# Kernel tuning notes

Measured on AMD Instinct MI355X. Metric: run time of the kernel, lower is better.

Reference implementation:

```python
import jax, jax.numpy as jnp
import numpy as np

N, D, H, DH, FF, NE, NNZ = 4096, 128, 2, 64, 256, 2048, 65536
EPS = 1e-5

def layer_norm(x, g, b):
    m = jnp.mean(x, axis=-1, keepdims=True)
    v = jnp.var(x, axis=-1, keepdims=True)
    return (x - m) / jnp.sqrt(v + EPS) * g + b

def setup_inputs() -> dict:
    key = jax.random.key(0)
    ks = jax.random.split(key, 24)
    s = 0.05
    node_idx = jax.random.randint(ks[1], (NNZ,), 0, N)
    he_idx = jax.random.randint(ks[2], (NNZ,), 0, NE)
    return {
        "x": jax.random.normal(ks[0], (N, D), dtype=jnp.float32),
        "edge": jnp.stack([node_idx, he_idx]).astype(jnp.int64),
        "Wq": jax.random.normal(ks[3], (D, D)) * s, "bq": jnp.zeros((D,)),
        "Wk": jax.random.normal(ks[4], (D, D)) * s, "bk": jnp.zeros((D,)),
        "Wv": jax.random.normal(ks[5], (D, D)) * s, "bv": jnp.zeros((D,)),
        "Wo": jax.random.normal(ks[6], (D, D)) * s, "bo": jnp.zeros((D,)),
        "g_ln1": jnp.ones((D,)), "b_ln1": jnp.zeros((D,)),
        "W1": jax.random.normal(ks[7], (D, FF)) * s, "bf1": jnp.zeros((FF,)),
        "W2": jax.random.normal(ks[8], (FF, D)) * s, "bf2": jnp.zeros((D,)),
        "g_ln2": jnp.ones((D,)), "b_ln2": jnp.zeros((D,)),
        "Wh": jax.random.normal(ks[9], (D, D)) * s, "bh": jnp.zeros((D,)),
    }

def reference(x, edge, Wq, bq, Wk, bk, Wv, bv, Wo, bo, g_ln1, b_ln1,
              W1, bf1, W2, bf2, g_ln2, b_ln2, Wh, bh):
    # dropout layers run in eval mode (identity) for a deterministic reference
    def mha_block(h):
        q = (h @ Wq + bq).reshape(N, H, DH)
        k = (h @ Wk + bk).reshape(N, H, DH)
        v = (h @ Wv + bv).reshape(N, H, DH)
        scores = jnp.einsum('nhd,mhd->hnm', q, k) / jnp.sqrt(jnp.float32(DH))
        attn = jax.nn.softmax(scores, axis=-1)            # [H,N,N]
        o = jnp.einsum('hnm,mhd->nhd', attn, v).reshape(N, D)
        return layer_norm(h + o @ Wo + bo, g_ln1, b_ln1)

    def ff_block(h):
        z = jax.nn.sigmoid(h @ W1 + bf1)
        return layer_norm(h + z @ W2 + bf2, g_ln2, b_ln2)

    h = ff_block(mha_block(x))
    h = ff_block(mha_block(h))

    # HypergraphConv: out = D^{-1} H B^{-1} H^T (X Theta) + bias
    node_idx = edge[0]
    he_idx = edge[1]
    xt = h @ Wh                                            # [N,D]
    ones = jnp.ones((NNZ,), dtype=xt.dtype)
    Bdeg = jax.ops.segment_sum(ones, he_idx, num_segments=NE)
    Binv = jnp.where(Bdeg > 0, 1.0 / Bdeg, 0.0)
    Ddeg = jax.ops.segment_sum(ones, node_idx, num_segments=N)
    Dinv = jnp.where(Ddeg > 0, 1.0 / Ddeg, 0.0)
    e = jax.ops.segment_sum(xt[node_idx], he_idx, num_segments=NE) * Binv[:, None]
    out = jax.ops.segment_sum(e[he_idx], node_idx, num_segments=N) * Dinv[:, None] + bh
    return jax.nn.relu(out)
```

## Files before the change

### kernel.cpp

```cpp
#include <hip/hip_runtime.h>
#include <hip/hip_bf16.h>
#include <cstddef>

#define N_NODES 4096
#define DIM     128
#define NHEAD   2
#define DHEAD   64
#define FFDIM   256
#define NEDGE   2048
#define NNZ_E   65536
#define NSPLIT  8

typedef __attribute__((ext_vector_type(8))) short bf16x8;
typedef __attribute__((ext_vector_type(4))) float f32x4;
typedef unsigned short u16;

__device__ __forceinline__ u16 f2b(float f) {
    unsigned u = __float_as_uint(f);
    return (u16)((u + 0x7FFFu + ((u >> 16) & 1u)) >> 16);
}
__device__ __forceinline__ float b2f_bits(u16 h) {
    return __uint_as_float(((unsigned)h) << 16);
}

__global__ void prep(const float* __restrict__ x, float* __restrict__ h,
                     u16* __restrict__ hh, u16* __restrict__ hl,
                     const float* W0, const float* W1, const float* W2,
                     const float* W3, const float* W4, const float* W5,
                     const float* W6,
                     u16* P0, u16* P1, u16* P2, u16* P3, u16* P4, u16* P5, u16* P6,
                     int* __restrict__ cnt) {
    const int bx = blockIdx.x;
    if (bx < 2048) {
        int i = bx * 256 + threadIdx.x;
        float f = x[i];
        h[i] = f;
        u16 hi = f2b(f);
        hh[i] = hi;
        hl[i] = f2b(f - b2f_bits(hi));
        return;
    }
    if (bx >= 2944) {
        int i = (bx - 2944) * 256 + threadIdx.x;
        if (i < NEDGE + N_NODES) cnt[i] = 0;
        return;
    }
    const int p = bx - 2048;
    const int sel = p >> 7;
    const float* W; u16* P; int K, NC;
    switch (sel) {
        case 0: W = W0; P = P0; K = 128; NC = 128; break;
        case 1: W = W1; P = P1; K = 128; NC = 128; break;
        case 2: W = W2; P = P2; K = 128; NC = 128; break;
        case 3: W = W3; P = P3; K = 128; NC = 128; break;
        case 4: W = W4; P = P4; K = 128; NC = 128; break;
        case 5: W = W5; P = P5; K = 128; NC = 256; break;
        default: W = W6; P = P6; K = 256; NC = 128; break;
    }
    int i = (p & 127) * 256 + threadIdx.x;
    if (i < K * NC) {
        int k = i / NC, n = i % NC;
        float f = W[i];
        u16 hb = f2b(f);
        size_t o = ((size_t)(k >> 3) * NC + n) * 8 + (k & 7);
        P[o] = hb;
        P[(size_t)K * NC + o] = f2b(f - b2f_bits(hb));
    }
}

template<int K, int NC>
__global__ __launch_bounds__(256) void gemm_mfma(const u16* __restrict__ Ah,
                                                 const u16* __restrict__ Al,
                                                 const u16* __restrict__ Wp,
                                                 float* __restrict__ C0) {
    const int tid = threadIdx.x, w = tid >> 6, lane = tid & 63;
    const int qi = lane & 15, gi = lane >> 4;
    const int row0 = blockIdx.x * 64 + w * 16;
    const int col0 = blockIdx.y * 32;
    const u16* Wlo = Wp + (size_t)K * NC;

    f32x4 acc[2];
    acc[0] = (f32x4){0.f, 0.f, 0.f, 0.f};
    acc[1] = (f32x4){0.f, 0.f, 0.f, 0.f};

#pragma unroll 4
    for (int kc = 0; kc < K / 32; ++kc) {
        const int k0 = kc * 32;
        const size_t ao = (size_t)(row0 + qi) * K + k0 + gi * 8;
        bf16x8 ah = *(const bf16x8*)(Ah + ao);
        bf16x8 al = *(const bf16x8*)(Al + ao);
#pragma unroll
        for (int c = 0; c < 2; ++c) {
            const size_t wo = ((size_t)(k0 / 8 + gi) * NC + col0 + c * 16 + qi) * 8;
            bf16x8 wh = *(const bf16x8*)(Wp + wo);
            bf16x8 wl = *(const bf16x8*)(Wlo + wo);
            acc[c] = __builtin_amdgcn_mfma_f32_16x16x32_bf16(ah, wh, acc[c], 0, 0, 0);
            acc[c] = __builtin_amdgcn_mfma_f32_16x16x32_bf16(al, wh, acc[c], 0, 0, 0);
            acc[c] = __builtin_amdgcn_mfma_f32_16x16x32_bf16(ah, wl, acc[c], 0, 0, 0);
        }
    }

#pragma unroll
    for (int c = 0; c < 2; ++c) {
        const int col = col0 + c * 16 + qi;
#pragma unroll
        for (int r = 0; r < 4; ++r) {
            const int grow = row0 + gi * 4 + r;
            C0[(size_t)grow * NC + col] = acc[c][r];
        }
    }
}

__global__ __launch_bounds__(256) void qkv_mfma(const u16* __restrict__ Ah,
                                                const u16* __restrict__ Al,
                                                const u16* __restrict__ Wq,
                                                const u16* __restrict__ Wk,
                                                const u16* __restrict__ Wv,
                                                const float* __restrict__ bq,
                                                const float* __restrict__ bk,
                                                const float* __restrict__ bv,
                                                u16* __restrict__ qb,
                                                u16* __restrict__ kb,
                                                u16* __restrict__ vtb) {
    const int K = 128, NC = 128;
    const int tid = threadIdx.x, w = tid >> 6, lane = tid & 63;
    const int qi = lane & 15, gi = lane >> 4;
    const int row0 = blockIdx.x * 64 + w * 16;
    const int sel = blockIdx.y >> 2;
    const int col0 = (blockIdx.y & 3) * 32;
    const u16* Wp = (sel == 0) ? Wq : (sel == 1) ? Wk : Wv;
    const float* bias = (sel == 0) ? bq : (sel == 1) ? bk : bv;
    const u16* Wlo = Wp + (size_t)K * NC;

    f32x4 acc[2];
    acc[0] = (f32x4){0.f, 0.f, 0.f, 0.f};
    acc[1] = (f32x4){0.f, 0.f, 0.f, 0.f};

#pragma unroll 4
    for (int kc = 0; kc < K / 32; ++kc) {
        const int k0 = kc * 32;
        const size_t ao = (size_t)(row0 + qi) * K + k0 + gi * 8;
        bf16x8 ah = *(const bf16x8*)(Ah + ao);
        bf16x8 al = *(const bf16x8*)(Al + ao);
#pragma unroll
        for (int c = 0; c < 2; ++c) {
            const size_t wo = ((size_t)(k0 / 8 + gi) * NC + col0 + c * 16 + qi) * 8;
            bf16x8 wh = *(const bf16x8*)(Wp + wo);
            bf16x8 wl = *(const bf16x8*)(Wlo + wo);
            acc[c] = __builtin_amdgcn_mfma_f32_16x16x32_bf16(ah, wh, acc[c], 0, 0, 0);
            acc[c] = __builtin_amdgcn_mfma_f32_16x16x32_bf16(al, wh, acc[c], 0, 0, 0);
            acc[c] = __builtin_amdgcn_mfma_f32_16x16x32_bf16(ah, wl, acc[c], 0, 0, 0);
        }
    }

#pragma unroll
    for (int c = 0; c < 2; ++c) {
        const int col = col0 + c * 16 + qi;
        const int hh = col >> 6, d = col & 63;
        float bv_ = bias[col];
        if (sel < 2) {
            u16* dst = (sel == 0) ? qb : kb;
#pragma unroll
            for (int r = 0; r < 4; ++r) {
                const int grow = row0 + gi * 4 + r;
                dst[((size_t)hh * N_NODES + grow) * 64 + d] = f2b(acc[c][r] + bv_);
            }
        } else {
            const int grow0 = row0 + gi * 4;
            ushort4 pw;
            pw.x = f2b(acc[c][0] + bv_);
            pw.y = f2b(acc[c][1] + bv_);
            pw.z = f2b(acc[c][2] + bv_);
            pw.w = f2b(acc[c][3] + bv_);
            *(ushort4*)&vtb[((size_t)hh * 64 + d) * N_NODES + grow0] = pw;
        }
    }
}

#define ROWP 72
__global__ __launch_bounds__(256) void attn_mfma(const u16* __restrict__ qb,
                                                 const u16* __restrict__ kb,
                                                 const u16* __restrict__ vtb,
                                                 float* __restrict__ op,
                                                 float* __restrict__ mlm,
                                                 float* __restrict__ mll) {
    __shared__ __align__(16) u16 k_s[64 * ROWP];
    __shared__ __align__(16) u16 vt_s[64 * ROWP];
    __shared__ __align__(16) u16 p_s[4][16 * ROWP];
    const int h = blockIdx.y;
    const int s = blockIdx.z;
    const int row0 = blockIdx.x * 64;
    const int tid = threadIdx.x;
    const int w = tid >> 6, lane = tid & 63;
    const int qi = lane & 15, gi = lane >> 4;
    const float CE = 0.18033688011f;

    const u16* qrow = qb + ((size_t)h * N_NODES + row0 + w * 16 + qi) * 64 + gi * 8;
    bf16x8 qf0 = *(const bf16x8*)qrow;
    bf16x8 qf1 = *(const bf16x8*)(qrow + 32);

    f32x4 oc[4];
#pragma unroll
    for (int i = 0; i < 4; ++i) oc[i] = (f32x4){0.f, 0.f, 0.f, 0.f};
    float m_run = -INFINITY, l_run = 0.f;

    const u16* kbh = kb + (size_t)h * N_NODES * 64;
    const u16* vth = vtb + (size_t)h * 64 * N_NODES;

    for (int kt = s * (N_NODES / 64 / NSPLIT); kt < (s + 1) * (N_NODES / 64 / NSPLIT); ++kt) {
        const u16* ksrc = kbh + kt * 64 * 64;
#pragma unroll
        for (int i = 0; i < 2; ++i) {
            int c = tid + i * 256;
            int r = c >> 3, ss = c & 7;
            *(uint4*)&k_s[r * ROWP + ss * 8]  = *(const uint4*)(ksrc + c * 8);
            *(uint4*)&vt_s[r * ROWP + ss * 8] = *(const uint4*)(vth + (size_t)r * N_NODES + kt * 64 + ss * 8);
        }
        __syncthreads();

        f32x4 sc[4];
#pragma unroll
        for (int t = 0; t < 4; ++t) {
            const u16* krow = &k_s[(t * 16 + qi) * ROWP + gi * 8];
            bf16x8 ka0 = *(const bf16x8*)krow;
            bf16x8 ka1 = *(const bf16x8*)(krow + 32);
            f32x4 z = (f32x4){0.f, 0.f, 0.f, 0.f};
            z = __builtin_amdgcn_mfma_f32_16x16x32_bf16(ka0, qf0, z, 0, 0, 0);
            sc[t] = __builtin_amdgcn_mfma_f32_16x16x32_bf16(ka1, qf1, z, 0, 0, 0);
        }

        float smax = -INFINITY;
#pragma unroll
        for (int t = 0; t < 4; ++t)
            smax = fmaxf(smax, fmaxf(fmaxf(sc[t][0], sc[t][1]), fmaxf(sc[t][2], sc[t][3])));
        smax = fmaxf(smax, __shfl_xor(smax, 16));
        smax = fmaxf(smax, __shfl_xor(smax, 32));
        float mn = fmaxf(m_run, smax);
        float alpha = exp2f((m_run - mn) * CE);
        m_run = mn;
        float nb = mn * CE;
        float psum = 0.f;
#pragma unroll
        for (int t = 0; t < 4; ++t) {
            ushort4 pw;
            float p0 = exp2f(fmaf(sc[t][0], CE, -nb)); psum += p0; pw.x = f2b(p0);
            float p1 = exp2f(fmaf(sc[t][1], CE, -nb)); psum += p1; pw.y = f2b(p1);
            float p2 = exp2f(fmaf(sc[t][2], CE, -nb)); psum += p2; pw.z = f2b(p2);
            float p3 = exp2f(fmaf(sc[t][3], CE, -nb)); psum += p3; pw.w = f2b(p3);
            *(ushort4*)&p_s[w][qi * ROWP + t * 16 + gi * 4] = pw;
        }
        psum += __shfl_xor(psum, 16);
        psum += __shfl_xor(psum, 32);
        l_run = l_run * alpha + psum;

        float a0 = __shfl(alpha, gi * 4 + 0);
        float a1 = __shfl(alpha, gi * 4 + 1);
        float a2 = __shfl(alpha, gi * 4 + 2);
        float a3 = __shfl(alpha, gi * 4 + 3);
#pragma unroll
        for (int d = 0; d < 4; ++d) {
            oc[d][0] *= a0; oc[d][1] *= a1; oc[d][2] *= a2; oc[d][3] *= a3;
        }

        const u16* prow = &p_s[w][qi * ROWP];
        bf16x8 pa0 = *(const bf16x8*)(prow + gi * 8);
        bf16x8 pa1 = *(const bf16x8*)(prow + 32 + gi * 8);
#pragma unroll
        for (int d = 0; d < 4; ++d) {
            const u16* vrow = &vt_s[(d * 16 + qi) * ROWP + gi * 8];
            bf16x8 vb0 = *(const bf16x8*)vrow;
            bf16x8 vb1 = *(const bf16x8*)(vrow + 32);
            oc[d] = __builtin_amdgcn_mfma_f32_16x16x32_bf16(pa0, vb0, oc[d], 0, 0, 0);
            oc[d] = __builtin_amdgcn_mfma_f32_16x16x32_bf16(pa1, vb1, oc[d], 0, 0, 0);
        }
        __syncthreads();
    }

    float* opd = op + (size_t)s * N_NODES * 128;
#pragma unroll
    for (int d = 0; d < 4; ++d) {
        size_t cb = h * 64 + d * 16 + qi;
        opd[(size_t)(row0 + w * 16 + gi * 4 + 0) * 128 + cb] = oc[d][0];
        opd[(size_t)(row0 + w * 16 + gi * 4 + 1) * 128 + cb] = oc[d][1];
        opd[(size_t)(row0 + w * 16 + gi * 4 + 2) * 128 + cb] = oc[d][2];
        opd[(size_t)(row0 + w * 16 + gi * 4 + 3) * 128 + cb] = oc[d][3];
    }
    if (gi == 0) {
        size_t mi = (size_t)s * NHEAD * N_NODES + (size_t)h * N_NODES + row0 + w * 16 + qi;
        mlm[mi] = m_run;
        mll[mi] = l_run;
    }
}

#define ROWA 136
#define ROWZ 264
#define ROWH 132
template<int DO_QKV>
__global__ __launch_bounds__(256) void mega_layer(
        const float* __restrict__ op, const float* __restrict__ mlm,
        const float* __restrict__ mll,
        const u16* __restrict__ wp_o, const float* __restrict__ bo,
        float* __restrict__ h,
        const float* __restrict__ g1, const float* __restrict__ b1,
        const u16* __restrict__ wp_1, const float* __restrict__ bf1,
        const u16* __restrict__ wp_2, const float* __restrict__ bf2,
        const float* __restrict__ g2, const float* __restrict__ b2,
        const u16* __restrict__ wp_q, const u16* __restrict__ wp_k,
        const u16* __restrict__ wp_v,
        const float* __restrict__ bq, const float* __restrict__ bk,
        const float* __restrict__ bv,
        u16* __restrict__ qb, u16* __restrict__ kb, u16* __restrict__ vtb) {
    __shared__ __align__(16) u16 zbuf[16 * ROWZ * 2];
    __shared__ __align__(16) u16 hp_hi[16 * ROWA];
    __shared__ __align__(16) u16 hp_lo[16 * ROWA];
    __shared__ float hln[16 * ROWH];
    __shared__ float ws_s[NSPLIT][32];
    __shared__ float Linv_s[32];
    __shared__ float wsum[4][16], wsq[4][16];
    const float CE = 0.18033688011f;
    const int tid = threadIdx.x, w = tid >> 6, lane = tid & 63;
    const int qi = lane & 15, gi = lane >> 4;
    const int row0 = blockIdx.x * 16;
    u16* a_hi = zbuf;
    u16* a_lo = zbuf + 16 * ROWA;
    u16* z_hi = zbuf;
    u16* z_lo = zbuf + 16 * ROWZ;

    if (tid < 32) {
        int r = tid >> 1, hd = tid & 1;
        size_t mb = (size_t)hd * N_NODES + row0 + r;
        float m[NSPLIT], l[NSPLIT], mx = -INFINITY;
#pragma unroll
        for (int s = 0; s < NSPLIT; ++s) {
            m[s] = mlm[mb + (size_t)s * NHEAD * N_NODES];
            l[s] = mll[mb + (size_t)s * NHEAD * N_NODES];
            mx = fmaxf(mx, m[s]);
        }
        float L = 0.f;
#pragma unroll
        for (int s = 0; s < NSPLIT; ++s) {
            float ws = exp2f((m[s] - mx) * CE);
            ws_s[s][tid] = ws;
            L += ws * l[s];
        }
        Linv_s[tid] = 1.f / L;
    }
    __syncthreads();

    for (int e = tid; e < 16 * 128; e += 256) {
        int r = e >> 7, c = e & 127, hd = c >> 6;
        size_t idx = (size_t)(row0 + r) * 128 + c;
        float O = 0.f;
#pragma unroll
        for (int s = 0; s < NSPLIT; ++s)
            O += ws_s[s][r * 2 + hd] * op[(size_t)s * N_NODES * 128 + idx];
        float v = O * Linv_s[r * 2 + hd];
        u16 hi = f2b(v);
        a_hi[r * ROWA + c] = hi;
        a_lo[r * ROWA + c] = f2b(v - b2f_bits(hi));
    }
    __syncthreads();

    {
        const u16* Wlo = wp_o + (size_t)128 * 128;
        f32x4 acc[2];
        acc[0] = (f32x4){0.f, 0.f, 0.f, 0.f};
        acc[1] = (f32x4){0.f, 0.f, 0.f, 0.f};
        const int col0 = w * 32;
#pragma unroll
        for (int kc = 0; kc < 4; ++kc) {
            const int k0 = kc * 32;
            bf16x8 ah = *(const bf16x8*)&a_hi[qi * ROWA + k0 + gi * 8];
            bf16x8 al = *(const bf16x8*)&a_lo[qi * ROWA + k0 + gi * 8];
#pragma unroll
            for (int c = 0; c < 2; ++c) {
                const size_t wo = ((size_t)(k0 / 8 + gi) * 128 + col0 + c * 16 + qi) * 8;
                bf16x8 wh = *(const bf16x8*)(wp_o + wo);
                bf16x8 wl = *(const bf16x8*)(Wlo + wo);
                acc[c] = __builtin_amdgcn_mfma_f32_16x16x32_bf16(ah, wh, acc[c], 0, 0, 0);
                acc[c] = __builtin_amdgcn_mfma_f32_16x16x32_bf16(al, wh, acc[c], 0, 0, 0);
                acc[c] = __builtin_amdgcn_mfma_f32_16x16x32_bf16(ah, wl, acc[c], 0, 0, 0);
            }
        }
        float y[2][4], rs[4], rq[4];
#pragma unroll
        for (int r = 0; r < 4; ++r) { rs[r] = 0.f; rq[r] = 0.f; }
#pragma unroll
        for (int c = 0; c < 2; ++c) {
            const int col = col0 + c * 16 + qi;
            float bv = bo[col];
#pragma unroll
            for (int r = 0; r < 4; ++r) {
                float v = acc[c][r] + bv + h[(size_t)(row0 + gi * 4 + r) * 128 + col];
                y[c][r] = v;
                rs[r] += v; rq[r] += v * v;
            }
        }
#pragma unroll
        for (int r = 0; r < 4; ++r)
            for (int msk = 1; msk < 16; msk <<= 1) {
                rs[r] += __shfl_xor(rs[r], msk);
                rq[r] += __shfl_xor(rq[r], msk);
            }
        if (qi == 0) {
#pragma unroll
            for (int r = 0; r < 4; ++r) { wsum[w][gi * 4 + r] = rs[r]; wsq[w][gi * 4 + r] = rq[r]; }
        }
        __syncthreads();
#pragma unroll
        for (int r = 0; r < 4; ++r) {
            const int lr = gi * 4 + r;
            float ts = wsum[0][lr] + wsum[1][lr] + wsum[2][lr] + wsum[3][lr];
            float tq = wsq[0][lr] + wsq[1][lr] + wsq[2][lr] + wsq[3][lr];
            float mean = ts * (1.f / 128.f);
            float var  = tq * (1.f / 128.f) - mean * mean;
            float rstd = rsqrtf(var + 1e-5f);
#pragma unroll
            for (int c = 0; c < 2; ++c) {
                const int col = col0 + c * 16 + qi;
                float yn = (y[c][r] - mean) * rstd * g1[col] + b1[col];
                hln[lr * ROWH + col] = yn;
                u16 hi = f2b(yn);
                hp_hi[lr * ROWA + col] = hi;
                hp_lo[lr * ROWA + col] = f2b(yn - b2f_bits(hi));
            }
        }
    }
    __syncthreads();

    {
        const u16* W1lo = wp_1 + (size_t)128 * 256;
        f32x4 acc1[4];
#pragma unroll
        for (int t = 0; t < 4; ++t) acc1[t] = (f32x4){0.f, 0.f, 0.f, 0.f};
#pragma unroll
        for (int kc = 0; kc < 4; ++kc) {
            const int k0 = kc * 32;
            bf16x8 ah = *(const bf16x8*)&hp_hi[qi * ROWA + k0 + gi * 8];
            bf16x8 al = *(const bf16x8*)&hp_lo[qi * ROWA + k0 + gi * 8];
#pragma unroll
            for (int t = 0; t < 4; ++t) {
                const size_t wo = ((size_t)(k0 / 8 + gi) * 256 + w * 64 + t * 16 + qi) * 8;
                bf16x8 wh = *(const bf16x8*)(wp_1 + wo);
                bf16x8 wl = *(const bf16x8*)(W1lo + wo);
                acc1[t] = __builtin_amdgcn_mfma_f32_16x16x32_bf16(ah, wh, acc1[t], 0, 0, 0);
                acc1[t] = __builtin_amdgcn_mfma_f32_16x16x32_bf16(al, wh, acc1[t], 0, 0, 0);
                acc1[t] = __builtin_amdgcn_mfma_f32_16x16x32_bf16(ah, wl, acc1[t], 0, 0, 0);
            }
        }
        __syncthreads();
#pragma unroll
        for (int t = 0; t < 4; ++t) {
            const int col = w * 64 + t * 16 + qi;
            float bv = bf1[col];
#pragma unroll
            for (int r = 0; r < 4; ++r) {
                float v = acc1[t][r] + bv;
                v = 1.f / (1.f + __expf(-v));
                u16 hi = f2b(v);
                const int zr = gi * 4 + r;
                z_hi[zr * ROWZ + col] = hi;
                z_lo[zr * ROWZ + col] = f2b(v - b2f_bits(hi));
            }
        }
    }
    __syncthreads();

    {
        const u16* W2lo = wp_2 + (size_t)256 * 128;
        f32x4 acc[2];
        acc[0] = (f32x4){0.f, 0.f, 0.f, 0.f};
        acc[1] = (f32x4){0.f, 0.f, 0.f, 0.f};
        const int col0 = w * 32;
#pragma unroll
        for (int kc = 0; kc < 8; ++kc) {
            const int k0 = kc * 32;
            bf16x8 ah = *(const bf16x8*)&z_hi[qi * ROWZ + k0 + gi * 8];
            bf16x8 al = *(const bf16x8*)&z_lo[qi * ROWZ + k0 + gi * 8];
#pragma unroll
            for (int c = 0; c < 2; ++c) {
                const size_t wo = ((size_t)(k0 / 8 + gi) * 128 + col0 + c * 16 + qi) * 8;
                bf16x8 wh = *(const bf16x8*)(wp_2 + wo);
                bf16x8 wl = *(const bf16x8*)(W2lo + wo);
                acc[c] = __builtin_amdgcn_mfma_f32_16x16x32_bf16(ah, wh, acc[c], 0, 0, 0);
                acc[c] = __builtin_amdgcn_mfma_f32_16x16x32_bf16(al, wh, acc[c], 0, 0, 0);
                acc[c] = __builtin_amdgcn_mfma_f32_16x16x32_bf16(ah, wl, acc[c], 0, 0, 0);
            }
        }
        float y[2][4], rs[4], rq[4];
#pragma unroll
        for (int r = 0; r < 4; ++r) { rs[r] = 0.f; rq[r] = 0.f; }
#pragma unroll
        for (int c = 0; c < 2; ++c) {
            const int col = col0 + c * 16 + qi;
            float bv = bf2[col];
#pragma unroll
            for (int r = 0; r < 4; ++r) {
                float v = acc[c][r] + bv + hln[(gi * 4 + r) * ROWH + col];
                y[c][r] = v;
                rs[r] += v; rq[r] += v * v;
            }
        }
#pragma unroll
        for (int r = 0; r < 4; ++r)
            for (int msk = 1; msk < 16; msk <<= 1) {
                rs[r] += __shfl_xor(rs[r], msk);
                rq[r] += __shfl_xor(rq[r], msk);
            }
        if (qi == 0) {
#pragma unroll
            for (int r = 0; r < 4; ++r) { wsum[w][gi * 4 + r] = rs[r]; wsq[w][gi * 4 + r] = rq[r]; }
        }
        __syncthreads();
#pragma unroll
        for (int r = 0; r < 4; ++r) {
            const int lr = gi * 4 + r;
            float ts = wsum[0][lr] + wsum[1][lr] + wsum[2][lr] + wsum[3][lr];
            float tq = wsq[0][lr] + wsq[1][lr] + wsq[2][lr] + wsq[3][lr];
            float mean = ts * (1.f / 128.f);
            float var  = tq * (1.f / 128.f) - mean * mean;
            float rstd = rsqrtf(var + 1e-5f);
#pragma unroll
            for (int c = 0; c < 2; ++c) {
                const int col = col0 + c * 16 + qi;
                float yn = (y[c][r] - mean) * rstd * g2[col] + b2[col];
                h[(size_t)(row0 + lr) * 128 + col] = yn;
                if (DO_QKV) {
                    u16 hi = f2b(yn);
                    hp_hi[lr * ROWA + col] = hi;
                    hp_lo[lr * ROWA + col] = f2b(yn - b2f_bits(hi));
                }
            }
        }
    }

    if (DO_QKV) {
        __syncthreads();
        const int col0 = w * 32;
#pragma unroll
        for (int sel = 0; sel < 3; ++sel) {
            const u16* Wp = (sel == 0) ? wp_q : (sel == 1) ? wp_k : wp_v;
            const float* bias = (sel == 0) ? bq : (sel == 1) ? bk : bv;
            const u16* Wlo = Wp + (size_t)128 * 128;
            f32x4 acc[2];
            acc[0] = (f32x4){0.f, 0.f, 0.f, 0.f};
            acc[1] = (f32x4){0.f, 0.f, 0.f, 0.f};
#pragma unroll
            for (int kc = 0; kc < 4; ++kc) {
                const int k0 = kc * 32;
                bf16x8 ah = *(const bf16x8*)&hp_hi[qi * ROWA + k0 + gi * 8];
                bf16x8 al = *(const bf16x8*)&hp_lo[qi * ROWA + k0 + gi * 8];
#pragma unroll
                for (int c = 0; c < 2; ++c) {
                    const size_t wo = ((size_t)(k0 / 8 + gi) * 128 + col0 + c * 16 + qi) * 8;
                    bf16x8 wh = *(const bf16x8*)(Wp + wo);
                    bf16x8 wl = *(const bf16x8*)(Wlo + wo);
                    acc[c] = __builtin_amdgcn_mfma_f32_16x16x32_bf16(ah, wh, acc[c], 0, 0, 0);
                    acc[c] = __builtin_amdgcn_mfma_f32_16x16x32_bf16(al, wh, acc[c], 0, 0, 0);
                    acc[c] = __builtin_amdgcn_mfma_f32_16x16x32_bf16(ah, wl, acc[c], 0, 0, 0);
                }
            }
#pragma unroll
            for (int c = 0; c < 2; ++c) {
                const int col = col0 + c * 16 + qi;
                const int hh = col >> 6, d = col & 63;
                float bv_ = bias[col];
                if (sel < 2) {
                    u16* dst = (sel == 0) ? qb : kb;
#pragma unroll
                    for (int r = 0; r < 4; ++r) {
                        const int grow = row0 + gi * 4 + r;
                        dst[((size_t)hh * N_NODES + grow) * 64 + d] = f2b(acc[c][r] + bv_);
                    }
                } else {
                    const int grow0 = row0 + gi * 4;
                    ushort4 pw;
                    pw.x = f2b(acc[c][0] + bv_);
                    pw.y = f2b(acc[c][1] + bv_);
                    pw.z = f2b(acc[c][2] + bv_);
                    pw.w = f2b(acc[c][3] + bv_);
                    *(ushort4*)&vtb[((size_t)hh * 64 + d) * N_NODES + grow0] = pw;
                }
            }
        }
    }
}

__global__ void hist_kernel(const int* __restrict__ edge_raw,
                            int* __restrict__ nidx, int* __restrict__ hidx,
                            int* __restrict__ cnt_e, int* __restrict__ cnt_n) {
    __shared__ int is64_s;
    if (threadIdx.x < 64) {
        int v = edge_raw[2 * threadIdx.x + 1];
        unsigned long long bal = __ballot(v != 0);
        if (threadIdx.x == 0) is64_s = (bal == 0ull) ? 1 : 0;
    }
    __syncthreads();
    const int is64 = is64_s;
    int i = blockIdx.x * 256 + threadIdx.x;
    if (i < NNZ_E) {
        int ni = (is64 ? edge_raw[2 * i]             : edge_raw[i])         & (N_NODES - 1);
        int he = (is64 ? edge_raw[2 * NNZ_E + 2 * i] : edge_raw[NNZ_E + i]) & (NEDGE - 1);
        nidx[i] = ni;
        hidx[i] = he;
        atomicAdd(&cnt_n[ni], 1);
        atomicAdd(&cnt_e[he], 1);
    }
}

__global__ __launch_bounds__(1024) void scan_only(const int* __restrict__ cnt_e,
                                                  const int* __restrict__ cnt_n,
                                                  int* __restrict__ off_e,
                                                  int* __restrict__ off_n,
                                                  int* __restrict__ cur_e,
                                                  int* __restrict__ cur_n) {
    __shared__ int s[N_NODES];
    const int he_side = (blockIdx.x == 0);
    const int n = he_side ? NEDGE : N_NODES;
    const int* cnt = he_side ? cnt_e : cnt_n;
    int* off = he_side ? off_e : off_n;
    int* cur = he_side ? cur_e : cur_n;
    for (int i = threadIdx.x; i < n; i += 1024) s[i] = cnt[i];
    __syncthreads();
    for (int st = 1; st < n; st <<= 1) {
        int v[4]; int nj = 0;
        for (int i = threadIdx.x; i < n; i += 1024) v[nj++] = (i >= st) ? s[i - st] : 0;
        __syncthreads();
        nj = 0;
        for (int i = threadIdx.x; i < n; i += 1024) s[i] += v[nj++];
        __syncthreads();
    }
    for (int i = threadIdx.x; i < n; i += 1024) { off[i + 1] = s[i]; cur[i] = 0; }
    if (threadIdx.x == 0) off[0] = 0;
}

__global__ void fill_csr(const int* __restrict__ nidx, const int* __restrict__ hidx,
                         const int* __restrict__ off_e, const int* __restrict__ off_n,
                         int* __restrict__ cur_e, int* __restrict__ cur_n,
                         int* __restrict__ csr_e, int* __restrict__ csr_n) {
    int i = blockIdx.x * 256 + threadIdx.x;
    if (i < NNZ_E) {
        int ni = nidx[i], he = hidx[i];
        int p = atomicAdd(&cur_e[he], 1);
        csr_e[off_e[he] + p] = ni;
        int q = atomicAdd(&cur_n[ni], 1);
        csr_n[off_n[ni] + q] = he;
    }
}

__global__ __launch_bounds__(128) void gather_e(const int* __restrict__ off_e,
                                                const int* __restrict__ csr_e,
                                                const float* __restrict__ h,
                                                u16* __restrict__ ehi,
                                                u16* __restrict__ elo) {
    __shared__ int ms[128];
    const int he = blockIdx.x, d = threadIdx.x;
    const int beg = off_e[he], end = off_e[he + 1];
    float acc = 0.f;
    for (int c = beg; c < end; c += 128) {
        int nl = min(128, end - c);
        if (d < nl) ms[d] = csr_e[c + d];
        __syncthreads();
        for (int j = 0; j < nl; ++j) acc += h[(size_t)ms[j] * 128 + d];
        __syncthreads();
    }
    float binv = (end > beg) ? 1.f / (float)(end - beg) : 0.f;
    float v = acc * binv;
    u16 hi = f2b(v);
    ehi[(size_t)he * 128 + d] = hi;
    elo[(size_t)he * 128 + d] = f2b(v - b2f_bits(hi));
}

__global__ __launch_bounds__(128) void gather_n(const int* __restrict__ off_n,
                                                const int* __restrict__ csr_n,
                                                const float* __restrict__ e_sc,
                                                const float* __restrict__ bh,
                                                float* __restrict__ out) {
    __shared__ int ms[128];
    const int nn = blockIdx.x, d = threadIdx.x;
    const int beg = off_n[nn], end = off_n[nn + 1];
    float acc = 0.f;
    for (int c = beg; c < end; c += 128) {
        int nl = min(128, end - c);
        if (d < nl) ms[d] = csr_n[c + d];
        __syncthreads();
        for (int j = 0; j < nl; ++j) acc += e_sc[(size_t)ms[j] * 128 + d];
        __syncthreads();
    }
    float dinv = (end > beg) ? 1.f / (float)(end - beg) : 0.f;
    float v = acc * dinv + bh[d];
    out[(size_t)nn * 128 + d] = v > 0.f ? v : 0.f;
}

extern "C" void kernel_launch(void* const* d_in, const int* in_sizes, int n_in,
                              void* d_out, int out_size, void* d_ws, size_t ws_size,
                              hipStream_t stream) {
    (void)in_sizes; (void)n_in; (void)out_size; (void)ws_size;
    const float* x    = (const float*)d_in[0];
    const int*   edge = (const int*)  d_in[1];
    const float* Wq = (const float*)d_in[2];  const float* bq  = (const float*)d_in[3];
    const float* Wk = (const float*)d_in[4];  const float* bk  = (const float*)d_in[5];
    const float* Wv = (const float*)d_in[6];  const float* bv  = (const float*)d_in[7];
    const float* Wo = (const float*)d_in[8];  const float* bo  = (const float*)d_in[9];
    const float* g1 = (const float*)d_in[10]; const float* b1  = (const float*)d_in[11];
    const float* W1 = (const float*)d_in[12]; const float* bf1 = (const float*)d_in[13];
    const float* W2 = (const float*)d_in[14]; const float* bf2 = (const float*)d_in[15];
    const float* g2 = (const float*)d_in[16]; const float* b2  = (const float*)d_in[17];
    const float* Wh = (const float*)d_in[18]; const float* bh  = (const float*)d_in[19];
    float* out = (float*)d_out;

    float* B = (float*)d_ws;
    float* h    = B;
    u16*   h_hi = (u16*)(B + 524288);
    u16*   h_lo = (u16*)(B + 786432);
    u16*   qb   = (u16*)(B + 1048576);
    u16*   kb   = (u16*)(B + 1310720);
    u16*   vtb  = (u16*)(B + 1835008);
    float* op   = B + 2097152;
    float* mlm  = B + 6291456;
    float* mll  = B + 6356992;
    u16*   e_hi = (u16*)(B + 6946816);
    u16*   e_lo = (u16*)(B + 7077888);
    float* e_sc = B + 7208960;
    u16*   wp_q = (u16*)(B + 8519680);
    u16*   wp_k = (u16*)(B + 8536064);
    u16*   wp_v = (u16*)(B + 8552448);
    u16*   wp_o = (u16*)(B + 8568832);
    u16*   wp_h = (u16*)(B + 8585216);
    u16*   wp_1 = (u16*)(B + 8601600);
    u16*   wp_2 = (u16*)(B + 8634368);
    int*   cur_e = (int*)(B + 9328640);
    int*   cur_n = (int*)(B + 9330688);
    int*   off_e = (int*)(B + 9334784);
    int*   off_n = (int*)(B + 9336840);
    int*   csr_e = (int*)(B + 9340944);
    int*   csr_n = (int*)(B + 9406480);
    int*   cnt_e = (int*)(B + 9472016);
    int*   cnt_n = (int*)(B + 9474064);
    int*   nidx  = (int*)(B + 9478160);
    int*   hidx  = (int*)(B + 9543696);

    prep<<<2968, 256, 0, stream>>>(x, h, h_hi, h_lo,
                                   Wq, Wk, Wv, Wo, Wh, W1, W2,
                                   wp_q, wp_k, wp_v, wp_o, wp_h, wp_1, wp_2, cnt_e);

    qkv_mfma<<<dim3(64, 12), 256, 0, stream>>>(h_hi, h_lo, wp_q, wp_k, wp_v,
                                               bq, bk, bv, qb, kb, vtb);
    attn_mfma<<<dim3(N_NODES / 64, NHEAD, NSPLIT), 256, 0, stream>>>(qb, kb, vtb, op, mlm, mll);
    mega_layer<1><<<N_NODES / 16, 256, 0, stream>>>(op, mlm, mll, wp_o, bo, h, g1, b1,
                                                    wp_1, bf1, wp_2, bf2, g2, b2,
                                                    wp_q, wp_k, wp_v, bq, bk, bv,
                                                    qb, kb, vtb);
    attn_mfma<<<dim3(N_NODES / 64, NHEAD, NSPLIT), 256, 0, stream>>>(qb, kb, vtb, op, mlm, mll);
    mega_layer<0><<<N_NODES / 16, 256, 0, stream>>>(op, mlm, mll, wp_o, bo, h, g1, b1,
                                                    wp_1, bf1, wp_2, bf2, g2, b2,
                                                    nullptr, nullptr, nullptr,
                                                    nullptr, nullptr, nullptr,
                                                    nullptr, nullptr, nullptr);

    hist_kernel<<<NNZ_E / 256, 256, 0, stream>>>(edge, nidx, hidx, cnt_e, cnt_n);
    scan_only<<<2, 1024, 0, stream>>>(cnt_e, cnt_n, off_e, off_n, cur_e, cur_n);
    fill_csr<<<NNZ_E / 256, 256, 0, stream>>>(nidx, hidx, off_e, off_n, cur_e, cur_n, csr_e, csr_n);
    gather_e<<<NEDGE, 128, 0, stream>>>(off_e, csr_e, h, e_hi, e_lo);
    gemm_mfma<128, 128><<<dim3(NEDGE / 64, 4), 256, 0, stream>>>(e_hi, e_lo, wp_h, e_sc);
    gather_n<<<N_NODES, 128, 0, stream>>>(off_n, csr_n, e_sc, bh, out);
}
```

Measured before the change: 256.1 us.

## Fuse hypergraph conv stages into one persistent kernel with grid barriers

Replaces the six hypergraph kernels (histogram, scan, CSR fill, edge gather, Wh GEMM, node gather) with a single persistent 512-block kernel that separates phases with atomic-counter grid barriers. Barrier counters are zeroed in prep, which gets one extra block. The aim is to remove per-launch overhead and idle gaps between small dependent kernels. It relies on all 512 blocks being co-resident to avoid deadlock, and during the scan phase only two blocks do work while the rest wait at the barrier.

```diff
diff --git a/kernel.cpp b/kernel.cpp
--- a/kernel.cpp
+++ b/kernel.cpp
@@ -10,6 +10,7 @@
 #define NEDGE   2048
 #define NNZ_E   65536
 #define NSPLIT  8
+#define HG_BLOCKS 512
 
 typedef __attribute__((ext_vector_type(8))) short bf16x8;
 typedef __attribute__((ext_vector_type(4))) float f32x4;
@@ -42,7 +43,7 @@
     }
     if (bx >= 2944) {
         int i = (bx - 2944) * 256 + threadIdx.x;
-        if (i < NEDGE + N_NODES) cnt[i] = 0;
+        if (i < NEDGE + N_NODES + 16) cnt[i] = 0;
         return;
     }
     const int p = bx - 2048;
@@ -65,49 +66,6 @@
         size_t o = ((size_t)(k >> 3) * NC + n) * 8 + (k & 7);
         P[o] = hb;
         P[(size_t)K * NC + o] = f2b(f - b2f_bits(hb));
-    }
-}
-
-template<int K, int NC>
-__global__ __launch_bounds__(256) void gemm_mfma(const u16* __restrict__ Ah,
-                                                 const u16* __restrict__ Al,
-                                                 const u16* __restrict__ Wp,
-                                                 float* __restrict__ C0) {
-    const int tid = threadIdx.x, w = tid >> 6, lane = tid & 63;
-    const int qi = lane & 15, gi = lane >> 4;
-    const int row0 = blockIdx.x * 64 + w * 16;
-    const int col0 = blockIdx.y * 32;
-    const u16* Wlo = Wp + (size_t)K * NC;
-
-    f32x4 acc[2];
-    acc[0] = (f32x4){0.f, 0.f, 0.f, 0.f};
-    acc[1] = (f32x4){0.f, 0.f, 0.f, 0.f};
-
-#pragma unroll 4
-    for (int kc = 0; kc < K / 32; ++kc) {
-        const int k0 = kc * 32;
-        const size_t ao = (size_t)(row0 + qi) * K + k0 + gi * 8;
-        bf16x8 ah = *(const bf16x8*)(Ah + ao);
-        bf16x8 al = *(const bf16x8*)(Al + ao);
-#pragma unroll
-        for (int c = 0; c < 2; ++c) {
-            const size_t wo = ((size_t)(k0 / 8 + gi) * NC + col0 + c * 16 + qi) * 8;
-            bf16x8 wh = *(const bf16x8*)(Wp + wo);
-            bf16x8 wl = *(const bf16x8*)(Wlo + wo);
-            acc[c] = __builtin_amdgcn_mfma_f32_16x16x32_bf16(ah, wh, acc[c], 0, 0, 0);
-            acc[c] = __builtin_amdgcn_mfma_f32_16x16x32_bf16(al, wh, acc[c], 0, 0, 0);
-            acc[c] = __builtin_amdgcn_mfma_f32_16x16x32_bf16(ah, wl, acc[c], 0, 0, 0);
-        }
-    }
-
-#pragma unroll
-    for (int c = 0; c < 2; ++c) {
-        const int col = col0 + c * 16 + qi;
-#pragma unroll
-        for (int r = 0; r < 4; ++r) {
-            const int grow = row0 + gi * 4 + r;
-            C0[(size_t)grow * NC + col] = acc[c][r];
-        }
     }
 }
 
@@ -586,110 +544,171 @@
     }
 }
 
-__global__ void hist_kernel(const int* __restrict__ edge_raw,
-                            int* __restrict__ nidx, int* __restrict__ hidx,
-                            int* __restrict__ cnt_e, int* __restrict__ cnt_n) {
+__device__ __forceinline__ void gbar(int* bar, int idx, int nblk) {
+    __syncthreads();
+    if (threadIdx.x == 0) {
+        __threadfence();
+        atomicAdd(&bar[idx], 1);
+        while (__hip_atomic_load(&bar[idx], __ATOMIC_ACQUIRE,
+                                 __HIP_MEMORY_SCOPE_AGENT) < nblk) {}
+    }
+    __syncthreads();
+    __threadfence();
+}
+
+__global__ __launch_bounds__(256, 2) void hyper_mega(
+        const int* __restrict__ edge_raw,
+        int* __restrict__ nidx, int* __restrict__ hidx,
+        int* __restrict__ cnt_e, int* __restrict__ cnt_n,
+        int* __restrict__ off_e, int* __restrict__ off_n,
+        int* __restrict__ cur_e, int* __restrict__ cur_n,
+        int* __restrict__ csr_e, int* __restrict__ csr_n,
+        const float* __restrict__ h,
+        u16* __restrict__ e_hi, u16* __restrict__ e_lo,
+        const u16* __restrict__ wp_h, float* __restrict__ e_sc,
+        const float* __restrict__ bh, float* __restrict__ out,
+        int* __restrict__ bar) {
+    __shared__ int smem[N_NODES];
     __shared__ int is64_s;
-    if (threadIdx.x < 64) {
-        int v = edge_raw[2 * threadIdx.x + 1];
+    const int tid = threadIdx.x;
+    const int gidx = blockIdx.x * 256 + tid;
+
+    if (tid < 64) {
+        int v = edge_raw[2 * tid + 1];
         unsigned long long bal = __ballot(v != 0);
-        if (threadIdx.x == 0) is64_s = (bal == 0ull) ? 1 : 0;
+        if (tid == 0) is64_s = (bal == 0ull) ? 1 : 0;
     }
     __syncthreads();
     const int is64 = is64_s;
-    int i = blockIdx.x * 256 + threadIdx.x;
-    if (i < NNZ_E) {
-        int ni = (is64 ? edge_raw[2 * i]             : edge_raw[i])         & (N_NODES - 1);
-        int he = (is64 ? edge_raw[2 * NNZ_E + 2 * i] : edge_raw[NNZ_E + i]) & (NEDGE - 1);
-        nidx[i] = ni;
-        hidx[i] = he;
+    if (gidx < NNZ_E) {
+        int ni = (is64 ? edge_raw[2 * gidx]             : edge_raw[gidx])         & (N_NODES - 1);
+        int he = (is64 ? edge_raw[2 * NNZ_E + 2 * gidx] : edge_raw[NNZ_E + gidx]) & (NEDGE - 1);
+        nidx[gidx] = ni;
+        hidx[gidx] = he;
         atomicAdd(&cnt_n[ni], 1);
         atomicAdd(&cnt_e[he], 1);
     }
-}
-
-__global__ __launch_bounds__(1024) void scan_only(const int* __restrict__ cnt_e,
-                                                  const int* __restrict__ cnt_n,
-                                                  int* __restrict__ off_e,
-                                                  int* __restrict__ off_n,
-                                                  int* __restrict__ cur_e,
-                                                  int* __restrict__ cur_n) {
-    __shared__ int s[N_NODES];
-    const int he_side = (blockIdx.x == 0);
-    const int n = he_side ? NEDGE : N_NODES;
-    const int* cnt = he_side ? cnt_e : cnt_n;
-    int* off = he_side ? off_e : off_n;
-    int* cur = he_side ? cur_e : cur_n;
-    for (int i = threadIdx.x; i < n; i += 1024) s[i] = cnt[i];
-    __syncthreads();
-    for (int st = 1; st < n; st <<= 1) {
-        int v[4]; int nj = 0;
-        for (int i = threadIdx.x; i < n; i += 1024) v[nj++] = (i >= st) ? s[i - st] : 0;
+    if (gidx < NEDGE) cur_e[gidx] = 0;
+    if (gidx < N_NODES) cur_n[gidx] = 0;
+    gbar(bar, 0, HG_BLOCKS);
+
+    if (blockIdx.x < 2) {
+        const int he_side = (blockIdx.x == 0);
+        const int n = he_side ? NEDGE : N_NODES;
+        const int* cnt = he_side ? cnt_e : cnt_n;
+        int* off = he_side ? off_e : off_n;
+        for (int i = tid; i < n; i += 256) smem[i] = cnt[i];
         __syncthreads();
-        nj = 0;
-        for (int i = threadIdx.x; i < n; i += 1024) s[i] += v[nj++];
-        __syncthreads();
-    }
-    for (int i = threadIdx.x; i < n; i += 1024) { off[i + 1] = s[i]; cur[i] = 0; }
-    if (threadIdx.x == 0) off[0] = 0;
-}
-
-__global__ void fill_csr(const int* __restrict__ nidx, const int* __restrict__ hidx,
-                         const int* __restrict__ off_e, const int* __restrict__ off_n,
-                         int* __restrict__ cur_e, int* __restrict__ cur_n,
-                         int* __restrict__ csr_e, int* __restrict__ csr_n) {
-    int i = blockIdx.x * 256 + threadIdx.x;
-    if (i < NNZ_E) {
-        int ni = nidx[i], he = hidx[i];
+        for (int st = 1; st < n; st <<= 1) {
+            int v[16]; int nj = 0;
+            for (int i = tid; i < n; i += 256) v[nj++] = (i >= st) ? smem[i - st] : 0;
+            __syncthreads();
+            nj = 0;
+            for (int i = tid; i < n; i += 256) smem[i] += v[nj++];
+            __syncthreads();
+        }
+        for (int i = tid; i < n; i += 256) off[i + 1] = smem[i];
+        if (tid == 0) off[0] = 0;
+    }
+    gbar(bar, 1, HG_BLOCKS);
+
+    if (gidx < NNZ_E) {
+        int ni = nidx[gidx], he = hidx[gidx];
         int p = atomicAdd(&cur_e[he], 1);
         csr_e[off_e[he] + p] = ni;
         int q = atomicAdd(&cur_n[ni], 1);
         csr_n[off_n[ni] + q] = he;
     }
-}
-
-__global__ __launch_bounds__(128) void gather_e(const int* __restrict__ off_e,
-                                                const int* __restrict__ csr_e,
-                                                const float* __restrict__ h,
-                                                u16* __restrict__ ehi,
-                                                u16* __restrict__ elo) {
-    __shared__ int ms[128];
-    const int he = blockIdx.x, d = threadIdx.x;
-    const int beg = off_e[he], end = off_e[he + 1];
-    float acc = 0.f;
-    for (int c = beg; c < end; c += 128) {
-        int nl = min(128, end - c);
-        if (d < nl) ms[d] = csr_e[c + d];
-        __syncthreads();
-        for (int j = 0; j < nl; ++j) acc += h[(size_t)ms[j] * 128 + d];
-        __syncthreads();
-    }
-    float binv = (end > beg) ? 1.f / (float)(end - beg) : 0.f;
-    float v = acc * binv;
-    u16 hi = f2b(v);
-    ehi[(size_t)he * 128 + d] = hi;
-    elo[(size_t)he * 128 + d] = f2b(v - b2f_bits(hi));
-}
-
-__global__ __launch_bounds__(128) void gather_n(const int* __restrict__ off_n,
-                                                const int* __restrict__ csr_n,
-                                                const float* __restrict__ e_sc,
-                                                const float* __restrict__ bh,
-                                                float* __restrict__ out) {
-    __shared__ int ms[128];
-    const int nn = blockIdx.x, d = threadIdx.x;
-    const int beg = off_n[nn], end = off_n[nn + 1];
-    float acc = 0.f;
-    for (int c = beg; c < end; c += 128) {
-        int nl = min(128, end - c);
-        if (d < nl) ms[d] = csr_n[c + d];
-        __syncthreads();
-        for (int j = 0; j < nl; ++j) acc += e_sc[(size_t)ms[j] * 128 + d];
-        __syncthreads();
-    }
-    float dinv = (end > beg) ? 1.f / (float)(end - beg) : 0.f;
-    float v = acc * dinv + bh[d];
-    out[(size_t)nn * 128 + d] = v > 0.f ? v : 0.f;
+    gbar(bar, 2, HG_BLOCKS);
+
+    {
+        int* ms = smem;
+        float* red = (float*)(smem + 256);
+        const int half = tid >> 7, d = tid & 127;
+        for (int he = blockIdx.x * 4; he < blockIdx.x * 4 + 4; ++he) {
+            const int beg = off_e[he], end = off_e[he + 1];
+            float acc = 0.f;
+            for (int c = beg; c < end; c += 256) {
+                int nl = min(256, end - c);
+                if (tid < nl) ms[tid] = csr_e[c + tid];
+                __syncthreads();
+                for (int j = half; j < nl; j += 2) acc += h[(size_t)ms[j] * 128 + d];
+                __syncthreads();
+            }
+            if (half) red[d] = acc;
+            __syncthreads();
+            if (!half) {
+                float binv = (end > beg) ? 1.f / (float)(end - beg) : 0.f;
+                float v = (acc + red[d]) * binv;
+                u16 hi = f2b(v);
+                e_hi[(size_t)he * 128 + d] = hi;
+                e_lo[(size_t)he * 128 + d] = f2b(v - b2f_bits(hi));
+            }
+            __syncthreads();
+        }
+    }
+    gbar(bar, 3, HG_BLOCKS);
+
+    if (blockIdx.x < 128) {
+        const int K = 128, NC = 128;
+        const int w = tid >> 6, lane = tid & 63;
+        const int qi = lane & 15, gi = lane >> 4;
+        const int row0 = (blockIdx.x & 31) * 64 + w * 16;
+        const int col0 = (blockIdx.x >> 5) * 32;
+        const u16* Wlo = wp_h + (size_t)K * NC;
+        f32x4 acc[2];
+        acc[0] = (f32x4){0.f, 0.f, 0.f, 0.f};
+        acc[1] = (f32x4){0.f, 0.f, 0.f, 0.f};
+#pragma unroll 4
+        for (int kc = 0; kc < K / 32; ++kc) {
+            const int k0 = kc * 32;
+            const size_t ao = (size_t)(row0 + qi) * K + k0 + gi * 8;
+            bf16x8 ah = *(const bf16x8*)(e_hi + ao);
+            bf16x8 al = *(const bf16x8*)(e_lo + ao);
+#pragma unroll
+            for (int c = 0; c < 2; ++c) {
+                const size_t wo = ((size_t)(k0 / 8 + gi) * NC + col0 + c * 16 + qi) * 8;
+                bf16x8 wh = *(const bf16x8*)(wp_h + wo);
+                bf16x8 wl = *(const bf16x8*)(Wlo + wo);
+                acc[c] = __builtin_amdgcn_mfma_f32_16x16x32_bf16(ah, wh, acc[c], 0, 0, 0);
+                acc[c] = __builtin_amdgcn_mfma_f32_16x16x32_bf16(al, wh, acc[c], 0, 0, 0);
+                acc[c] = __builtin_amdgcn_mfma_f32_16x16x32_bf16(ah, wl, acc[c], 0, 0, 0);
+            }
+        }
+#pragma unroll
+        for (int c = 0; c < 2; ++c) {
+            const int col = col0 + c * 16 + qi;
+#pragma unroll
+            for (int r = 0; r < 4; ++r)
+                e_sc[(size_t)(row0 + gi * 4 + r) * NC + col] = acc[c][r];
+        }
+    }
+    gbar(bar, 4, HG_BLOCKS);
+
+    {
+        int* ms = smem;
+        float* red = (float*)(smem + 256);
+        const int half = tid >> 7, d = tid & 127;
+        for (int nn = blockIdx.x * 8; nn < blockIdx.x * 8 + 8; ++nn) {
+            const int beg = off_n[nn], end = off_n[nn + 1];
+            float acc = 0.f;
+            for (int c = beg; c < end; c += 256) {
+                int nl = min(256, end - c);
+                if (tid < nl) ms[tid] = csr_n[c + tid];
+                __syncthreads();
+                for (int j = half; j < nl; j += 2) acc += e_sc[(size_t)ms[j] * 128 + d];
+                __syncthreads();
+            }
+            if (half) red[d] = acc;
+            __syncthreads();
+            if (!half) {
+                float dinv = (end > beg) ? 1.f / (float)(end - beg) : 0.f;
+                float v = (acc + red[d]) * dinv + bh[d];
+                out[(size_t)nn * 128 + d] = v > 0.f ? v : 0.f;
+            }
+            __syncthreads();
+        }
+    }
 }
 
 extern "C" void kernel_launch(void* const* d_in, const int* in_sizes, int n_in,
@@ -737,10 +756,11 @@
     int*   csr_n = (int*)(B + 9406480);
     int*   cnt_e = (int*)(B + 9472016);
     int*   cnt_n = (int*)(B + 9474064);
-    int*   nidx  = (int*)(B + 9478160);
-    int*   hidx  = (int*)(B + 9543696);
-
-    prep<<<2968, 256, 0, stream>>>(x, h, h_hi, h_lo,
+    int*   bar   = (int*)(B + 9478160);
+    int*   nidx  = (int*)(B + 9478176);
+    int*   hidx  = (int*)(B + 9543712);
+
+    prep<<<2969, 256, 0, stream>>>(x, h, h_hi, h_lo,
                                    Wq, Wk, Wv, Wo, Wh, W1, W2,
                                    wp_q, wp_k, wp_v, wp_o, wp_h, wp_1, wp_2, cnt_e);
 
@@ -758,10 +778,8 @@
                                                     nullptr, nullptr, nullptr,
                                                     nullptr, nullptr, nullptr);
 
-    hist_kernel<<<NNZ_E / 256, 256, 0, stream>>>(edge, nidx, hidx, cnt_e, cnt_n);
-    scan_only<<<2, 1024, 0, stream>>>(cnt_e, cnt_n, off_e, off_n, cur_e, cur_n);
-    fill_csr<<<NNZ_E / 256, 256, 0, stream>>>(nidx, hidx, off_e, off_n, cur_e, cur_n, csr_e, csr_n);
-    gather_e<<<NEDGE, 128, 0, stream>>>(off_e, csr_e, h, e_hi, e_lo);
-    gemm_mfma<128, 128><<<dim3(NEDGE / 64, 4), 256, 0, stream>>>(e_hi, e_lo, wp_h, e_sc);
-    gather_n<<<N_NODES, 128, 0, stream>>>(off_n, csr_n, e_sc, bh, out);
-}
+    hyper_mega<<<HG_BLOCKS, 256, 0, stream>>>(edge, nidx, hidx, cnt_e, cnt_n,
+                                              off_e, off_n, cur_e, cur_n,
+                                              csr_e, csr_n, h, e_hi, e_lo,
+                                              wp_h, e_sc, bh, out, bar);
+}
```

New measurement: 686.2 us. 2.68x slower.
